# Optimization experiments

Hardware: AMD Instinct MI355X
Metric: run time of the kernel (lower is better)

Reference implementation:

```python
import jax, jax.numpy as jnp
import numpy as np

B, S, D, H = 2, 2048, 1024, 16


def setup_inputs() -> dict:
    key = jax.random.key(0)
    kq, kk, kv, kw = jax.random.split(key, 4)
    Q = jax.random.normal(kq, (B, S, D), dtype=jnp.float32)
    K = jax.random.normal(kk, (B, S, D), dtype=jnp.float32)
    V = jax.random.normal(kv, (B, S, D), dtype=jnp.float32)
    Wo = jax.random.normal(kw, (D, D), dtype=jnp.float32) * (1.0 / np.sqrt(D))
    return {"Q": Q, "K": K, "V": V, "Wo": Wo, "num_heads": H}


def reference(Q, K, V, Wo, num_heads):
    b, s, d = Q.shape
    dk = d // num_heads
    # split heads: [B,S,D] -> [B,H,S,dk]
    q = Q.reshape(b, s, num_heads, dk).transpose(0, 2, 1, 3)
    k = K.reshape(b, s, num_heads, dk).transpose(0, 2, 1, 3)
    v = V.reshape(b, s, num_heads, dk).transpose(0, 2, 1, 3)
    scale = 1.0 / jnp.sqrt(jnp.asarray(dk, dtype=q.dtype))
    logits = jnp.einsum('bhqd,bhkd->bhqk', q, k) * scale  # [B,H,S,S]
    probs = jax.nn.softmax(logits, axis=-1).astype(q.dtype)
    o = jnp.einsum('bhqk,bhkd->bhqd', probs, v)  # [B,H,S,dk]
    o = o.transpose(0, 2, 1, 3).reshape(b, s, d)  # concat heads
    # O = einsum('d dkh, ... dkh -> ... d', Wo, scores) == scores @ Wo^T
    return jnp.einsum('dk,bsk->bsd', Wo, o)
```

## Files before the change

### kernel.cpp

```cpp
#include <hip/hip_runtime.h>
#include <hip/hip_bf16.h>

#define B_ 2
#define S_ 2048
#define D_ 1024
#define H_ 16
#define DK_ 64

typedef __hip_bfloat16 bf16;
typedef short v8s __attribute__((ext_vector_type(8)));
typedef short v4s __attribute__((ext_vector_type(4)));
typedef float v4f __attribute__((ext_vector_type(4)));
typedef float v16f __attribute__((ext_vector_type(16)));
typedef int   v4i __attribute__((ext_vector_type(4)));

static __device__ __forceinline__ v4f mfma16(v8s a, v8s b, v4f c) {
  return __builtin_amdgcn_mfma_f32_16x16x32_bf16(a, b, c, 0, 0, 0);
}
static __device__ __forceinline__ v16f mfma32(v8s a, v8s b, v16f c) {
  return __builtin_amdgcn_mfma_f32_32x32x16_bf16(a, b, c, 0, 0, 0);
}
static __device__ __forceinline__ void gl2lds16(const void* g, void* l) {
  __builtin_amdgcn_global_load_lds((const __attribute__((address_space(1))) void*)g,
                                   (__attribute__((address_space(3))) void*)l,
                                   16, 0, 0);
}
static __device__ __forceinline__ unsigned short bfb(float x) {
  return __builtin_bit_cast(unsigned short, __float2bfloat16(x));
}
static __device__ __forceinline__ short f2bf(float x) { return (short)bfb(x); }
static __device__ __forceinline__ int pk2(float lo, float hi) {
  return (int)(((unsigned)bfb(hi) << 16) | (unsigned)bfb(lo));
}

__global__ __launch_bounds__(256) void cvt_k_kernel(const float* __restrict__ K,
                                                    bf16* __restrict__ Kb) {
  const int idx = blockIdx.x * 256 + threadIdx.x;
  const int seg = idx & 7;
  const int rest = idx >> 3;
  const int h = rest & 15;
  const int bs = rest >> 4;
  const float* src = K + (size_t)bs * D_ + h * 64 + seg * 8;
  v4f x = *(const v4f*)src, y = *(const v4f*)(src + 4);
  v8s r;
  r[0]=f2bf(x[0]); r[1]=f2bf(x[1]); r[2]=f2bf(x[2]); r[3]=f2bf(x[3]);
  r[4]=f2bf(y[0]); r[5]=f2bf(y[1]); r[6]=f2bf(y[2]); r[7]=f2bf(y[3]);
  const int b = bs >> 11, s = bs & 2047;
  *(v8s*)(Kb + ((size_t)(b * H_ + h) * S_ + s) * DK_ + seg * 8) = r;
}

__global__ __launch_bounds__(256) void tv_kernel(const float* __restrict__ V,
                                                 bf16* __restrict__ Vt) {
  __shared__ __align__(16) bf16 td[64 * 72];
  const int t = threadIdx.x;
  const int bh = blockIdx.x, b = bh >> 4, h = bh & 15;
  const int s0 = blockIdx.y * 64;
  const int srow = t >> 2;
  const int cs = t & 3;
  const float* vp = V + (size_t)(b * S_ + s0 + srow) * D_ + h * 64 + cs * 16;
#pragma unroll
  for (int j = 0; j < 4; j++) {
    v4f x = *(const v4f*)(vp + j * 4);
#pragma unroll
    for (int jj = 0; jj < 4; jj++)
      td[(cs * 16 + j * 4 + jj) * 72 + srow] = __float2bfloat16(x[jj]);
  }
  __syncthreads();
  const int d = t >> 2, sseg = t & 3;
#pragma unroll
  for (int j = 0; j < 2; j++) {
    v8s val = *(const v8s*)(td + d * 72 + sseg * 16 + j * 8);
    *(v8s*)(Vt + ((size_t)bh * DK_ + d) * S_ + s0 + sseg * 16 + j * 8) = val;
  }
}

__global__ __launch_bounds__(256) void cvt_wo_kernel(const float* __restrict__ Wo,
                                                     bf16* __restrict__ Wb) {
  const int i = (blockIdx.x * 256 + threadIdx.x) * 4;
  v4f a = *(const v4f*)(Wo + i);
  v4s r;
  r[0]=f2bf(a[0]); r[1]=f2bf(a[1]); r[2]=f2bf(a[2]); r[3]=f2bf(a[3]);
  *(v4s*)((short*)Wb + i) = r;
}

__global__ __launch_bounds__(256, 2) void attn2_kernel(
    const float* __restrict__ Q, const bf16* __restrict__ Kb,
    const bf16* __restrict__ Vt, bf16* __restrict__ Ow)
{
  __shared__ __align__(16) bf16 kk[2][32 * 64];
  __shared__ __align__(16) bf16 vv[2][64 * 32];
  __shared__ __align__(16) bf16 ep[4][32 * 72];

  const int t = threadIdx.x;
  const int w = t >> 6;
  const int l = t & 63;
  const int h2 = l >> 5;
  const int ln = l & 31;

  const int bh = blockIdx.x;
  const int b = bh >> 4, h = bh & 15;
  const int qbase = blockIdx.y * 128 + w * 32;

  const bf16* Kbh = Kb + (size_t)bh * (S_ * DK_);
  const bf16* Vbh = Vt + (size_t)bh * (DK_ * S_);

  const int krow = t >> 3, ksrc_seg = (t & 7) ^ (krow & 7);
  const int vrow = t >> 2, vsrc_seg = (t & 3) ^ (vrow & 3);

  const float sc = 0.18033688011112042f;
  v8s bq[4];
  {
    const float* qp = Q + ((size_t)b * S_ + qbase + ln) * D_ + h * DK_ + h2 * 8;
#pragma unroll
    for (int c = 0; c < 4; c++) {
      v4f x = *(const v4f*)(qp + c * 16);
      v4f y = *(const v4f*)(qp + c * 16 + 4);
      v8s r;
      r[0]=f2bf(x[0]*sc); r[1]=f2bf(x[1]*sc); r[2]=f2bf(x[2]*sc); r[3]=f2bf(x[3]*sc);
      r[4]=f2bf(y[0]*sc); r[5]=f2bf(y[1]*sc); r[6]=f2bf(y[2]*sc); r[7]=f2bf(y[3]*sc);
      bq[c] = r;
    }
  }

  v16f accA, accB;
#pragma unroll
  for (int r = 0; r < 16; r++) { accA[r] = 0.f; accB[r] = 0.f; }
  float lpart = 0.f;

  gl2lds16(Kbh + (size_t)krow * DK_ + ksrc_seg * 8, &kk[0][t * 8]);
  gl2lds16(Vbh + (size_t)vrow * S_ + vsrc_seg * 8, &vv[0][t * 8]);

  int it = 0;
  for (int kb = 0; kb < S_; kb += 32, it ^= 1) {
    __syncthreads();
    if (kb + 32 < S_) {
      gl2lds16(Kbh + (size_t)(kb + 32 + krow) * DK_ + ksrc_seg * 8, &kk[it ^ 1][t * 8]);
      gl2lds16(Vbh + (size_t)vrow * S_ + (kb + 32) + vsrc_seg * 8, &vv[it ^ 1][t * 8]);
    }
    const bf16* kc_ = kk[it];
    const bf16* vc_ = vv[it];

    v16f s;
#pragma unroll
    for (int r = 0; r < 16; r++) s[r] = 0.f;
#pragma unroll
    for (int c = 0; c < 4; c++) {
      const int sd = 2 * c + h2;
      v8s ak = *(const v8s*)(kc_ + ln * 64 + ((sd ^ (ln & 7)) * 8));
      s = mfma32(ak, bq[c], s);
    }

    float p[16];
#pragma unroll
    for (int r = 0; r < 16; r++) p[r] = exp2f(s[r]);
    float su = 0.f;
#pragma unroll
    for (int r = 0; r < 16; r++) su += p[r];
    lpart += su;

    int Pk[8], Sw[8];
#pragma unroll
    for (int g = 0; g < 8; g++) Pk[g] = pk2(p[2 * g], p[2 * g + 1]);
#pragma unroll
    for (int g = 0; g < 8; g++) Sw[g] = __shfl_xor(Pk[g], 32);

    v4i b0i, b1i;
    b0i[0] = h2 ? Sw[2] : Pk[0];  b0i[1] = h2 ? Sw[3] : Pk[1];
    b0i[2] = h2 ? Pk[2] : Sw[0];  b0i[3] = h2 ? Pk[3] : Sw[1];
    b1i[0] = h2 ? Sw[6] : Pk[4];  b1i[1] = h2 ? Sw[7] : Pk[5];
    b1i[2] = h2 ? Pk[6] : Sw[4];  b1i[3] = h2 ? Pk[7] : Sw[5];
    v8s pb0 = __builtin_bit_cast(v8s, b0i);
    v8s pb1 = __builtin_bit_cast(v8s, b1i);

#pragma unroll
    for (int kc = 0; kc < 2; kc++) {
      const int sk = 2 * kc + h2;
      const int dA = ln;
      const int dB = 32 + ln;
      v8s avA = *(const v8s*)(vc_ + dA * 32 + ((sk ^ (dA & 3)) * 8));
      v8s avB = *(const v8s*)(vc_ + dB * 32 + ((sk ^ (dB & 3)) * 8));
      accA = mfma32(avA, kc ? pb1 : pb0, accA);
      accB = mfma32(avB, kc ? pb1 : pb0, accB);
    }
  }

  const float linv = 1.0f / (lpart + __shfl_xor(lpart, 32));
  bf16* epw = ep[w];
#pragma unroll
  for (int r = 0; r < 16; r++) {
    const int dr = (r & 3) + 8 * (r >> 2) + 4 * h2;
    epw[ln * 72 + dr]      = __float2bfloat16(accA[r] * linv);
    epw[ln * 72 + 32 + dr] = __float2bfloat16(accB[r] * linv);
  }
  __syncthreads();
#pragma unroll
  for (int i = 0; i < 4; i++) {
    const int flat = i * 64 + l;
    const int qr = flat >> 3, seg = flat & 7;
    v8s val = *(const v8s*)(epw + qr * 72 + seg * 8);
    const int srow = qbase - w * 32 + w * 32 + qr;
    *(v8s*)(Ow + ((size_t)b * S_ + qbase + qr) * D_ + h * DK_ + seg * 8) = val;
    (void)srow;
  }
}

__global__ __launch_bounds__(256, 2) void proj2_kernel(
    const bf16* __restrict__ A, const bf16* __restrict__ Wo, float* __restrict__ Out)
{
  __shared__ __align__(16) bf16 aa[2][64 * 32];
  __shared__ __align__(16) bf16 bb[2][128 * 32];

  const int t = threadIdx.x;
  const int w = t >> 6;
  const int l = t & 63;
  const int quad = l >> 4;
  const int lm = l & 15;

  const int m0 = blockIdx.x * 64;
  const int n0 = blockIdx.y * 128;
  const int wm = (w & 1) * 32;
  const int wn = (w >> 1) * 64;

  v4f acc[2][4];
#pragma unroll
  for (int i = 0; i < 2; i++)
#pragma unroll
    for (int j = 0; j < 4; j++)
      acc[i][j] = {0.f, 0.f, 0.f, 0.f};

  const int arow = t >> 2, aseg = t & 3;

  gl2lds16(A + (size_t)(m0 + arow) * D_ + aseg * 8, &aa[0][t * 8]);
#pragma unroll
  for (int j = 0; j < 2; j++) {
    const int flat = j * 256 + t;
    gl2lds16(Wo + (size_t)(n0 + (flat >> 2)) * D_ + (flat & 3) * 8, &bb[0][flat * 8]);
  }

  int it = 0;
  for (int k0 = 0; k0 < D_; k0 += 32, it ^= 1) {
    __syncthreads();
    if (k0 + 32 < D_) {
      gl2lds16(A + (size_t)(m0 + arow) * D_ + (k0 + 32) + aseg * 8, &aa[it ^ 1][t * 8]);
#pragma unroll
      for (int j = 0; j < 2; j++) {
        const int flat = j * 256 + t;
        gl2lds16(Wo + (size_t)(n0 + (flat >> 2)) * D_ + (k0 + 32) + (flat & 3) * 8,
                 &bb[it ^ 1][flat * 8]);
      }
    }
    const bf16* ac = aa[it];
    const bf16* bc = bb[it];

    v8s am[2], bn[4];
#pragma unroll
    for (int i = 0; i < 2; i++)
      am[i] = *(const v8s*)(ac + (wm + i * 16 + lm) * 32 + quad * 8);
#pragma unroll
    for (int i = 0; i < 4; i++)
      bn[i] = *(const v8s*)(bc + (wn + i * 16 + lm) * 32 + quad * 8);
#pragma unroll
    for (int mi = 0; mi < 2; mi++)
#pragma unroll
      for (int ni = 0; ni < 4; ni++)
        acc[mi][ni] = mfma16(am[mi], bn[ni], acc[mi][ni]);
  }

#pragma unroll
  for (int mi = 0; mi < 2; mi++) {
#pragma unroll
    for (int r = 0; r < 4; r++) {
      const int row = m0 + wm + mi * 16 + quad * 4 + r;
      float* orow = Out + (size_t)row * D_ + n0 + wn + lm;
#pragma unroll
      for (int ni = 0; ni < 4; ni++)
        orow[ni * 16] = acc[mi][ni][r];
    }
  }
}

extern "C" void kernel_launch(void* const* d_in, const int* in_sizes, int n_in,
                              void* d_out, int out_size, void* d_ws, size_t ws_size,
                              hipStream_t stream) {
  (void)in_sizes; (void)n_in; (void)out_size; (void)ws_size;
  const float* Q  = (const float*)d_in[0];
  const float* K  = (const float*)d_in[1];
  const float* V  = (const float*)d_in[2];
  const float* Wo = (const float*)d_in[3];
  float* out = (float*)d_out;

  bf16* kb   = (bf16*)d_ws;
  bf16* vt   = kb + (size_t)4 * 1024 * 1024;
  bf16* ows  = vt + (size_t)4 * 1024 * 1024;
  bf16* wo_b = ows + (size_t)4 * 1024 * 1024;

  cvt_k_kernel <<<dim3(2048),     256, 0, stream>>>(K, kb);
  tv_kernel    <<<dim3(32, 32),   256, 0, stream>>>(V, vt);
  cvt_wo_kernel<<<dim3(1024),     256, 0, stream>>>(Wo, wo_b);
  attn2_kernel <<<dim3(32, 16),   256, 0, stream>>>(Q, kb, vt, ows);
  proj2_kernel <<<dim3(64, 8),    256, 0, stream>>>(ows, wo_b, out);
}
```

Before: 200.1 us.

## Permute V transpose layout to drop P shuffles and widen key tiles

The V transpose kernel now writes key positions in a permuted order that matches the MFMA output register layout. This lets the attention kernel feed packed probabilities straight into the PV MFMA without cross-half shuffles. The attention loop processes 64 keys per iteration with swizzled K/V LDS tiles, bf16 packing uses a cheaper perm-based round, and the epilogue stores packed pairs with a swizzle. The projection GEMM switches to 32x32 MFMA tiles with 64x64 blocks and k-step 64. The risks are higher register and LDS pressure, and the rounding mode changes from exact round-to-nearest-even to round-half-up.

```diff
diff --git a/kernel.cpp b/kernel.cpp
--- a/kernel.cpp
+++ b/kernel.cpp
@@ -14,9 +14,6 @@
 typedef float v16f __attribute__((ext_vector_type(16)));
 typedef int   v4i __attribute__((ext_vector_type(4)));
 
-static __device__ __forceinline__ v4f mfma16(v8s a, v8s b, v4f c) {
-  return __builtin_amdgcn_mfma_f32_16x16x32_bf16(a, b, c, 0, 0, 0);
-}
 static __device__ __forceinline__ v16f mfma32(v8s a, v8s b, v16f c) {
   return __builtin_amdgcn_mfma_f32_32x32x16_bf16(a, b, c, 0, 0, 0);
 }
@@ -25,12 +22,13 @@
                                    (__attribute__((address_space(3))) void*)l,
                                    16, 0, 0);
 }
-static __device__ __forceinline__ unsigned short bfb(float x) {
-  return __builtin_bit_cast(unsigned short, __float2bfloat16(x));
-}
-static __device__ __forceinline__ short f2bf(float x) { return (short)bfb(x); }
-static __device__ __forceinline__ int pk2(float lo, float hi) {
-  return (int)(((unsigned)bfb(hi) << 16) | (unsigned)bfb(lo));
+static __device__ __forceinline__ short f2bf(float x) {
+  return (short)__builtin_bit_cast(unsigned short, __float2bfloat16(x));
+}
+static __device__ __forceinline__ int pk2f(float lo, float hi) {
+  unsigned a = __builtin_bit_cast(unsigned, lo) + 0x8000u;
+  unsigned b = __builtin_bit_cast(unsigned, hi) + 0x8000u;
+  return (int)__builtin_amdgcn_perm(b, a, 0x07060302u);
 }
 
 __global__ __launch_bounds__(256) void cvt_k_kernel(const float* __restrict__ K,
@@ -66,11 +64,15 @@
       td[(cs * 16 + j * 4 + jj) * 72 + srow] = __float2bfloat16(x[jj]);
   }
   __syncthreads();
-  const int d = t >> 2, sseg = t & 3;
-#pragma unroll
-  for (int j = 0; j < 2; j++) {
-    v8s val = *(const v8s*)(td + d * 72 + sseg * 16 + j * 8);
-    *(v8s*)(Vt + ((size_t)bh * DK_ + d) * S_ + s0 + sseg * 16 + j * 8) = val;
+  const int d = t >> 2;
+#pragma unroll
+  for (int a2 = 0; a2 < 4; a2++) {
+    const int pos = cs * 16 + a2 * 4;
+    const int g = pos >> 5;
+    const int a = (pos >> 2) & 7;
+    const int kbase = g * 32 + ((a >> 2) << 4) + ((a & 1) << 3) + (((a >> 1) & 1) << 2);
+    v4s val = *(const v4s*)(td + d * 72 + kbase);
+    *(v4s*)(Vt + ((size_t)bh * DK_ + d) * S_ + s0 + pos) = val;
   }
 }
 
@@ -83,29 +85,21 @@
   *(v4s*)((short*)Wb + i) = r;
 }
 
-__global__ __launch_bounds__(256, 2) void attn2_kernel(
+__global__ __launch_bounds__(256, 2) void attn3_kernel(
     const float* __restrict__ Q, const bf16* __restrict__ Kb,
     const bf16* __restrict__ Vt, bf16* __restrict__ Ow)
 {
-  __shared__ __align__(16) bf16 kk[2][32 * 64];
-  __shared__ __align__(16) bf16 vv[2][64 * 32];
+  __shared__ __align__(16) bf16 kk[2][64 * 64];
+  __shared__ __align__(16) bf16 vv[2][64 * 64];
   __shared__ __align__(16) bf16 ep[4][32 * 72];
 
   const int t = threadIdx.x;
-  const int w = t >> 6;
-  const int l = t & 63;
-  const int h2 = l >> 5;
-  const int ln = l & 31;
-
-  const int bh = blockIdx.x;
-  const int b = bh >> 4, h = bh & 15;
+  const int w = t >> 6, l = t & 63, h2 = l >> 5, ln = l & 31;
+  const int bh = blockIdx.x, b = bh >> 4, h = bh & 15;
   const int qbase = blockIdx.y * 128 + w * 32;
 
   const bf16* Kbh = Kb + (size_t)bh * (S_ * DK_);
   const bf16* Vbh = Vt + (size_t)bh * (DK_ * S_);
-
-  const int krow = t >> 3, ksrc_seg = (t & 7) ^ (krow & 7);
-  const int vrow = t >> 2, vsrc_seg = (t & 3) ^ (vrow & 3);
 
   const float sc = 0.18033688011112042f;
   v8s bq[4];
@@ -115,10 +109,9 @@
     for (int c = 0; c < 4; c++) {
       v4f x = *(const v4f*)(qp + c * 16);
       v4f y = *(const v4f*)(qp + c * 16 + 4);
-      v8s r;
-      r[0]=f2bf(x[0]*sc); r[1]=f2bf(x[1]*sc); r[2]=f2bf(x[2]*sc); r[3]=f2bf(x[3]*sc);
-      r[4]=f2bf(y[0]*sc); r[5]=f2bf(y[1]*sc); r[6]=f2bf(y[2]*sc); r[7]=f2bf(y[3]*sc);
-      bq[c] = r;
+      v4i r = { pk2f(x[0]*sc, x[1]*sc), pk2f(x[2]*sc, x[3]*sc),
+                pk2f(y[0]*sc, y[1]*sc), pk2f(y[2]*sc, y[3]*sc) };
+      bq[c] = __builtin_bit_cast(v8s, r);
     }
   }
 
@@ -127,155 +120,146 @@
   for (int r = 0; r < 16; r++) { accA[r] = 0.f; accB[r] = 0.f; }
   float lpart = 0.f;
 
-  gl2lds16(Kbh + (size_t)krow * DK_ + ksrc_seg * 8, &kk[0][t * 8]);
-  gl2lds16(Vbh + (size_t)vrow * S_ + vsrc_seg * 8, &vv[0][t * 8]);
+#pragma unroll
+  for (int j = 0; j < 2; j++) {
+    const int flat = j * 256 + t, row = flat >> 3, sp = flat & 7;
+    gl2lds16(Kbh + (size_t)row * DK_ + ((sp ^ (row & 7)) * 8), &kk[0][flat * 8]);
+    gl2lds16(Vbh + (size_t)row * S_ + ((sp ^ (row & 7)) * 8), &vv[0][flat * 8]);
+  }
 
   int it = 0;
-  for (int kb = 0; kb < S_; kb += 32, it ^= 1) {
+  for (int kb = 0; kb < S_; kb += 64, it ^= 1) {
     __syncthreads();
-    if (kb + 32 < S_) {
-      gl2lds16(Kbh + (size_t)(kb + 32 + krow) * DK_ + ksrc_seg * 8, &kk[it ^ 1][t * 8]);
-      gl2lds16(Vbh + (size_t)vrow * S_ + (kb + 32) + vsrc_seg * 8, &vv[it ^ 1][t * 8]);
+    if (kb + 64 < S_) {
+#pragma unroll
+      for (int j = 0; j < 2; j++) {
+        const int flat = j * 256 + t, row = flat >> 3, sp = flat & 7;
+        gl2lds16(Kbh + (size_t)(kb + 64 + row) * DK_ + ((sp ^ (row & 7)) * 8),
+                 &kk[it ^ 1][flat * 8]);
+        gl2lds16(Vbh + (size_t)row * S_ + (kb + 64) + ((sp ^ (row & 7)) * 8),
+                 &vv[it ^ 1][flat * 8]);
+      }
     }
     const bf16* kc_ = kk[it];
     const bf16* vc_ = vv[it];
 
-    v16f s;
-#pragma unroll
-    for (int r = 0; r < 16; r++) s[r] = 0.f;
+    v16f s0, s1;
+#pragma unroll
+    for (int r = 0; r < 16; r++) { s0[r] = 0.f; s1[r] = 0.f; }
 #pragma unroll
     for (int c = 0; c < 4; c++) {
       const int sd = 2 * c + h2;
-      v8s ak = *(const v8s*)(kc_ + ln * 64 + ((sd ^ (ln & 7)) * 8));
-      s = mfma32(ak, bq[c], s);
-    }
-
-    float p[16];
-#pragma unroll
-    for (int r = 0; r < 16; r++) p[r] = exp2f(s[r]);
+      v8s a0 = *(const v8s*)(kc_ + ln * 64 + ((sd ^ (ln & 7)) * 8));
+      v8s a1 = *(const v8s*)(kc_ + (32 + ln) * 64 + ((sd ^ (ln & 7)) * 8));
+      s0 = mfma32(a0, bq[c], s0);
+      s1 = mfma32(a1, bq[c], s1);
+    }
+
+    float p0[16], p1[16];
+#pragma unroll
+    for (int r = 0; r < 16; r++) { p0[r] = exp2f(s0[r]); p1[r] = exp2f(s1[r]); }
     float su = 0.f;
 #pragma unroll
-    for (int r = 0; r < 16; r++) su += p[r];
+    for (int r = 0; r < 16; r++) su += p0[r] + p1[r];
     lpart += su;
 
-    int Pk[8], Sw[8];
-#pragma unroll
-    for (int g = 0; g < 8; g++) Pk[g] = pk2(p[2 * g], p[2 * g + 1]);
-#pragma unroll
-    for (int g = 0; g < 8; g++) Sw[g] = __shfl_xor(Pk[g], 32);
-
-    v4i b0i, b1i;
-    b0i[0] = h2 ? Sw[2] : Pk[0];  b0i[1] = h2 ? Sw[3] : Pk[1];
-    b0i[2] = h2 ? Pk[2] : Sw[0];  b0i[3] = h2 ? Pk[3] : Sw[1];
-    b1i[0] = h2 ? Sw[6] : Pk[4];  b1i[1] = h2 ? Sw[7] : Pk[5];
-    b1i[2] = h2 ? Pk[6] : Sw[4];  b1i[3] = h2 ? Pk[7] : Sw[5];
-    v8s pb0 = __builtin_bit_cast(v8s, b0i);
-    v8s pb1 = __builtin_bit_cast(v8s, b1i);
-
-#pragma unroll
-    for (int kc = 0; kc < 2; kc++) {
-      const int sk = 2 * kc + h2;
-      const int dA = ln;
-      const int dB = 32 + ln;
-      v8s avA = *(const v8s*)(vc_ + dA * 32 + ((sk ^ (dA & 3)) * 8));
-      v8s avB = *(const v8s*)(vc_ + dB * 32 + ((sk ^ (dB & 3)) * 8));
-      accA = mfma32(avA, kc ? pb1 : pb0, accA);
-      accB = mfma32(avB, kc ? pb1 : pb0, accB);
-    }
-  }
-
-  const float linv = 1.0f / (lpart + __shfl_xor(lpart, 32));
+    v4i i00 = { pk2f(p0[0],p0[1]),  pk2f(p0[2],p0[3]),  pk2f(p0[4],p0[5]),  pk2f(p0[6],p0[7]) };
+    v4i i01 = { pk2f(p0[8],p0[9]),  pk2f(p0[10],p0[11]),pk2f(p0[12],p0[13]),pk2f(p0[14],p0[15]) };
+    v4i i10 = { pk2f(p1[0],p1[1]),  pk2f(p1[2],p1[3]),  pk2f(p1[4],p1[5]),  pk2f(p1[6],p1[7]) };
+    v4i i11 = { pk2f(p1[8],p1[9]),  pk2f(p1[10],p1[11]),pk2f(p1[12],p1[13]),pk2f(p1[14],p1[15]) };
+    v8s pb00 = __builtin_bit_cast(v8s, i00);
+    v8s pb01 = __builtin_bit_cast(v8s, i01);
+    v8s pb10 = __builtin_bit_cast(v8s, i10);
+    v8s pb11 = __builtin_bit_cast(v8s, i11);
+
+#pragma unroll
+    for (int st = 0; st < 2; st++) {
+#pragma unroll
+      for (int kc = 0; kc < 2; kc++) {
+        const int q = st * 4 + kc * 2 + h2;
+        v8s avA = *(const v8s*)(vc_ + ln * 64 + ((q ^ (ln & 7)) * 8));
+        v8s avB = *(const v8s*)(vc_ + (32 + ln) * 64 + ((q ^ (ln & 7)) * 8));
+        v8s pb = st ? (kc ? pb11 : pb10) : (kc ? pb01 : pb00);
+        accA = mfma32(avA, pb, accA);
+        accB = mfma32(avB, pb, accB);
+      }
+    }
+  }
+
+  const float lfull = lpart + __shfl_xor(lpart, 32);
+  const float linv = 1.0f / lfull;
   bf16* epw = ep[w];
-#pragma unroll
-  for (int r = 0; r < 16; r++) {
-    const int dr = (r & 3) + 8 * (r >> 2) + 4 * h2;
-    epw[ln * 72 + dr]      = __float2bfloat16(accA[r] * linv);
-    epw[ln * 72 + 32 + dr] = __float2bfloat16(accB[r] * linv);
+  const int swz = (ln >> 3) & 3;
+#pragma unroll
+  for (int r = 0; r < 16; r += 2) {
+    const int off = (r & 3) + 4 * h2;
+    const int spA = (r >> 2) ^ swz;
+    const int vA = pk2f(accA[r] * linv, accA[r + 1] * linv);
+    const int vB = pk2f(accB[r] * linv, accB[r + 1] * linv);
+    *(int*)(epw + ln * 72 + spA * 8 + off) = vA;
+    *(int*)(epw + ln * 72 + (4 + spA) * 8 + off) = vB;
   }
   __syncthreads();
 #pragma unroll
   for (int i = 0; i < 4; i++) {
     const int flat = i * 64 + l;
-    const int qr = flat >> 3, seg = flat & 7;
-    v8s val = *(const v8s*)(epw + qr * 72 + seg * 8);
-    const int srow = qbase - w * 32 + w * 32 + qr;
-    *(v8s*)(Ow + ((size_t)b * S_ + qbase + qr) * D_ + h * DK_ + seg * 8) = val;
-    (void)srow;
-  }
-}
-
-__global__ __launch_bounds__(256, 2) void proj2_kernel(
+    const int qr = flat >> 3, sd = flat & 7;
+    const int pos = 4 * (sd >> 2) + ((sd & 3) ^ ((qr >> 3) & 3));
+    v8s val = *(const v8s*)(epw + qr * 72 + pos * 8);
+    *(v8s*)(Ow + ((size_t)b * S_ + qbase + qr) * D_ + h * DK_ + sd * 8) = val;
+  }
+}
+
+__global__ __launch_bounds__(256, 4) void proj3_kernel(
     const bf16* __restrict__ A, const bf16* __restrict__ Wo, float* __restrict__ Out)
 {
-  __shared__ __align__(16) bf16 aa[2][64 * 32];
-  __shared__ __align__(16) bf16 bb[2][128 * 32];
+  __shared__ __align__(16) bf16 aa[2][64 * 64];
+  __shared__ __align__(16) bf16 bb[2][64 * 64];
 
   const int t = threadIdx.x;
-  const int w = t >> 6;
-  const int l = t & 63;
-  const int quad = l >> 4;
-  const int lm = l & 15;
-
-  const int m0 = blockIdx.x * 64;
-  const int n0 = blockIdx.y * 128;
-  const int wm = (w & 1) * 32;
-  const int wn = (w >> 1) * 64;
-
-  v4f acc[2][4];
-#pragma unroll
-  for (int i = 0; i < 2; i++)
-#pragma unroll
-    for (int j = 0; j < 4; j++)
-      acc[i][j] = {0.f, 0.f, 0.f, 0.f};
-
-  const int arow = t >> 2, aseg = t & 3;
-
-  gl2lds16(A + (size_t)(m0 + arow) * D_ + aseg * 8, &aa[0][t * 8]);
+  const int w = t >> 6, l = t & 63, h2 = l >> 5, ln = l & 31;
+  const int m0 = blockIdx.x * 64, n0 = blockIdx.y * 64;
+  const int wm = (w & 1) * 32, wn = (w >> 1) * 32;
+
+  v16f acc;
+#pragma unroll
+  for (int r = 0; r < 16; r++) acc[r] = 0.f;
+
 #pragma unroll
   for (int j = 0; j < 2; j++) {
-    const int flat = j * 256 + t;
-    gl2lds16(Wo + (size_t)(n0 + (flat >> 2)) * D_ + (flat & 3) * 8, &bb[0][flat * 8]);
+    const int flat = j * 256 + t, row = flat >> 3, sp = flat & 7;
+    gl2lds16(A  + (size_t)(m0 + row) * D_ + ((sp ^ (row & 7)) * 8), &aa[0][flat * 8]);
+    gl2lds16(Wo + (size_t)(n0 + row) * D_ + ((sp ^ (row & 7)) * 8), &bb[0][flat * 8]);
   }
 
   int it = 0;
-  for (int k0 = 0; k0 < D_; k0 += 32, it ^= 1) {
+  for (int k0 = 0; k0 < D_; k0 += 64, it ^= 1) {
     __syncthreads();
-    if (k0 + 32 < D_) {
-      gl2lds16(A + (size_t)(m0 + arow) * D_ + (k0 + 32) + aseg * 8, &aa[it ^ 1][t * 8]);
+    if (k0 + 64 < D_) {
 #pragma unroll
       for (int j = 0; j < 2; j++) {
-        const int flat = j * 256 + t;
-        gl2lds16(Wo + (size_t)(n0 + (flat >> 2)) * D_ + (k0 + 32) + (flat & 3) * 8,
+        const int flat = j * 256 + t, row = flat >> 3, sp = flat & 7;
+        gl2lds16(A  + (size_t)(m0 + row) * D_ + (k0 + 64) + ((sp ^ (row & 7)) * 8),
+                 &aa[it ^ 1][flat * 8]);
+        gl2lds16(Wo + (size_t)(n0 + row) * D_ + (k0 + 64) + ((sp ^ (row & 7)) * 8),
                  &bb[it ^ 1][flat * 8]);
       }
     }
     const bf16* ac = aa[it];
     const bf16* bc = bb[it];
-
-    v8s am[2], bn[4];
-#pragma unroll
-    for (int i = 0; i < 2; i++)
-      am[i] = *(const v8s*)(ac + (wm + i * 16 + lm) * 32 + quad * 8);
-#pragma unroll
-    for (int i = 0; i < 4; i++)
-      bn[i] = *(const v8s*)(bc + (wn + i * 16 + lm) * 32 + quad * 8);
-#pragma unroll
-    for (int mi = 0; mi < 2; mi++)
-#pragma unroll
-      for (int ni = 0; ni < 4; ni++)
-        acc[mi][ni] = mfma16(am[mi], bn[ni], acc[mi][ni]);
-  }
-
-#pragma unroll
-  for (int mi = 0; mi < 2; mi++) {
-#pragma unroll
-    for (int r = 0; r < 4; r++) {
-      const int row = m0 + wm + mi * 16 + quad * 4 + r;
-      float* orow = Out + (size_t)row * D_ + n0 + wn + lm;
-#pragma unroll
-      for (int ni = 0; ni < 4; ni++)
-        orow[ni * 16] = acc[mi][ni][r];
-    }
+#pragma unroll
+    for (int c = 0; c < 4; c++) {
+      const int sd = 2 * c + h2;
+      v8s av = *(const v8s*)(ac + (wm + ln) * 64 + ((sd ^ (ln & 7)) * 8));
+      v8s bv = *(const v8s*)(bc + (wn + ln) * 64 + ((sd ^ (ln & 7)) * 8));
+      acc = mfma32(av, bv, acc);
+    }
+  }
+
+#pragma unroll
+  for (int r = 0; r < 16; r++) {
+    const int row = m0 + wm + (r & 3) + 4 * h2 + 8 * (r >> 2);
+    Out[(size_t)row * D_ + n0 + wn + ln] = acc[r];
   }
 }
 
@@ -294,9 +278,9 @@
   bf16* ows  = vt + (size_t)4 * 1024 * 1024;
   bf16* wo_b = ows + (size_t)4 * 1024 * 1024;
 
-  cvt_k_kernel <<<dim3(2048),     256, 0, stream>>>(K, kb);
-  tv_kernel    <<<dim3(32, 32),   256, 0, stream>>>(V, vt);
-  cvt_wo_kernel<<<dim3(1024),     256, 0, stream>>>(Wo, wo_b);
-  attn2_kernel <<<dim3(32, 16),   256, 0, stream>>>(Q, kb, vt, ows);
-  proj2_kernel <<<dim3(64, 8),    256, 0, stream>>>(ows, wo_b, out);
-}
+  cvt_k_kernel <<<dim3(2048),   256, 0, stream>>>(K, kb);
+  tv_kernel    <<<dim3(32, 32), 256, 0, stream>>>(V, vt);
+  cvt_wo_kernel<<<dim3(1024),   256, 0, stream>>>(Wo, wo_b);
+  attn3_kernel <<<dim3(32, 16), 256, 0, stream>>>(Q, kb, vt, ows);
+  proj3_kernel <<<dim3(64, 16), 256, 0, stream>>>(ows, wo_b, out);
+}
```

Result: faster. 178.1 us (-11.0%).
